# Kernel tuning notes

Hardware: AMD Instinct MI355X
Metric: run time of the kernel (lower is better)

Reference implementation:

```python
import jax, jax.numpy as jnp
import numpy as np

B, T, D, H, HD, E, F, K = 512, 32, 512, 16, 32, 4, 2048, 2
EPS = 1e-5

def gelu_gpt2(x):
    c = np.sqrt(2.0 / np.pi).astype(np.float32)
    return 0.5 * x * (1.0 + jnp.tanh(c * (x + 0.044715 * x ** 3)))

def layernorm(x, g, b):
    m = jnp.mean(x, axis=-1, keepdims=True)
    v = jnp.mean((x - m) ** 2, axis=-1, keepdims=True)
    return (x - m) * jax.lax.rsqrt(v + EPS) * g + b

def setup_inputs() -> dict:
    key = jax.random.key(0)
    ks = jax.random.split(key, 12)
    s = 0.02
    return {
        "x": jax.random.normal(ks[0], (B, T, D), jnp.float32),
        "ln1_g": jnp.ones((D,), jnp.float32), "ln1_b": jnp.zeros((D,), jnp.float32),
        "wq": jax.random.normal(ks[1], (H, D, HD), jnp.float32) * s,
        "wk": jax.random.normal(ks[2], (H, D, HD), jnp.float32) * s,
        "wv": jax.random.normal(ks[3], (H, D, HD), jnp.float32) * s,
        "w_proj": jax.random.normal(ks[4], (D, D), jnp.float32) * s,
        "b_proj": jnp.zeros((D,), jnp.float32),
        "ln2_g": jnp.ones((D,), jnp.float32), "ln2_b": jnp.zeros((D,), jnp.float32),
        "w_gate": jax.random.normal(ks[5], (D, E), jnp.float32) * s,
        "w1": jax.random.normal(ks[6], (E, D, F), jnp.float32) * s,
        "b1": jnp.zeros((E, F), jnp.float32),
        "w2": jax.random.normal(ks[7], (E, F, D), jnp.float32) * s,
        "b2": jnp.zeros((E, D), jnp.float32),
    }

def reference(x, ln1_g, ln1_b, wq, wk, wv, w_proj, b_proj, ln2_g, ln2_b, w_gate, w1, b1, w2, b2):
    # --- multi-head causal attention (dropout = eval-mode identity) ---
    h = layernorm(x, ln1_g, ln1_b)                       # [B,T,D]
    q = jnp.einsum('btd,hde->bhte', h, wq)
    k = jnp.einsum('btd,hde->bhte', h, wk)
    v = jnp.einsum('btd,hde->bhte', h, wv)
    # NOTE: original scales by 1/sqrt(n_embd), not head_size
    wei = jnp.einsum('bhte,bhse->bhts', q, k) / jnp.sqrt(jnp.float32(D))
    mask = jnp.tril(jnp.ones((T, T), bool))
    wei = jnp.where(mask, wei, -jnp.inf)
    wei = jax.nn.softmax(wei, axis=-1)
    att = jnp.einsum('bhts,bhse->bhte', wei, v)          # [B,H,T,HD]
    att = att.transpose(0, 2, 1, 3).reshape(B, T, D)     # concat heads
    x = x + att @ w_proj + b_proj
    # --- mixture of experts FFN ---
    h2 = layernorm(x, ln2_g, ln2_b).reshape(-1, D)       # [N,D]
    logits = h2 @ w_gate                                  # [N,E] raw gate output
    # faithful to original: scalar mean over all logits
    ep = jnp.mean(logits)
    bal_loss = ep * jnp.log(ep + 0.1)
    w_top, sel = jax.lax.top_k(logits, K)                # [N,K]
    w_top = jax.nn.softmax(w_top, axis=-1)
    combine = jnp.sum(w_top[:, :, None] * jax.nn.one_hot(sel, E, dtype=x.dtype), axis=1)  # [N,E]
    mid = gelu_gpt2(jnp.einsum('nd,edf->nef', h2, w1) + b1)   # [N,E,F]
    eout = jnp.einsum('nef,efd->ned', mid, w2) + b2           # [N,E,D]
    moe = jnp.einsum('ne,ned->nd', combine, eout).reshape(B, T, D)
    return (x + moe, bal_loss)
```

## Files before the change

### kernel.cpp

```cpp
#include <hip/hip_runtime.h>

typedef unsigned short ushort;
typedef unsigned int   uint;
typedef short bf16x8 __attribute__((ext_vector_type(8)));
typedef float f32x4  __attribute__((ext_vector_type(4)));

__device__ __forceinline__ float bf2f(ushort u){
  union { uint u; float f; } c; c.u = ((uint)u) << 16; return c.f;
}
__device__ __forceinline__ ushort f2bf(float f){
  union { float f; uint u; } c; c.f = f;
  return (ushort)((c.u + 0x7fffu + ((c.u >> 16) & 1u)) >> 16);
}
__device__ __forceinline__ float wredsum(float v){
  #pragma unroll
  for (int off = 32; off > 0; off >>= 1) v += __shfl_xor(v, off);
  return v;
}
__device__ __forceinline__ void gload16(const void* g, void* l){
  __builtin_amdgcn_global_load_lds((__attribute__((address_space(1))) void*)(void*)g,
                                   (__attribute__((address_space(3))) void*)l, 16, 0, 0);
}

template<bool SPLIT>
__global__ __launch_bounds__(256) void transpose_to_bf16(
    const float* __restrict__ src, ushort* __restrict__ dhi, ushort* __restrict__ dlo,
    int R, int C)
{
  __shared__ float tile[32][33];
  size_t zoff = (size_t)blockIdx.z * R * C;
  src += zoff; dhi += zoff; if (SPLIT) dlo += zoff;
  int c0 = blockIdx.x * 32, r0 = blockIdx.y * 32;
  int tx = threadIdx.x & 31, ty = threadIdx.x >> 5;
  #pragma unroll
  for (int i = 0; i < 32; i += 8)
    tile[ty + i][tx] = src[(size_t)(r0 + ty + i) * C + (c0 + tx)];
  __syncthreads();
  #pragma unroll
  for (int i = 0; i < 32; i += 8){
    float v = tile[tx][ty + i];
    ushort hi = f2bf(v);
    dhi[(size_t)(c0 + ty + i) * R + (r0 + tx)] = hi;
    if constexpr (SPLIT)
      dlo[(size_t)(c0 + ty + i) * R + (r0 + tx)] = f2bf(v - bf2f(hi));
  }
}

__global__ __launch_bounds__(256) void transpose_qkv(
    const float* __restrict__ wq, const float* __restrict__ wk, const float* __restrict__ wv,
    ushort* __restrict__ dhi, ushort* __restrict__ dlo)
{
  __shared__ float tile[32][33];
  int z = blockIdx.z;
  int which = z >> 4, h = z & 15;
  const float* src = (which == 0) ? wq : (which == 1) ? wk : wv;
  size_t soff = (size_t)h * 512 * 32;
  size_t doff = (size_t)which * 262144 + soff;
  src += soff;
  int r0 = blockIdx.y * 32;
  int tx = threadIdx.x & 31, ty = threadIdx.x >> 5;
  #pragma unroll
  for (int i = 0; i < 32; i += 8)
    tile[ty + i][tx] = src[(size_t)(r0 + ty + i) * 32 + tx];
  __syncthreads();
  #pragma unroll
  for (int i = 0; i < 32; i += 8){
    float v = tile[tx][ty + i];
    ushort hi = f2bf(v);
    dhi[doff + (size_t)(ty + i) * 512 + (r0 + tx)] = hi;
    dlo[doff + (size_t)(ty + i) * 512 + (r0 + tx)] = f2bf(v - bf2f(hi));
  }
}

__global__ __launch_bounds__(256) void ln_split(
    const float* __restrict__ x, const float* __restrict__ g, const float* __restrict__ b,
    ushort* __restrict__ hhi, ushort* __restrict__ hlo)
{
  int w = threadIdx.x >> 6, lane = threadIdx.x & 63;
  int row = blockIdx.x * 4 + w;
  const float* xr = x + (size_t)row * 512;
  int d = lane * 8;
  float4 a0 = *(const float4*)(xr + d);
  float4 a1 = *(const float4*)(xr + d + 4);
  float v[8] = {a0.x,a0.y,a0.z,a0.w,a1.x,a1.y,a1.z,a1.w};
  float s = 0.f;
  #pragma unroll
  for (int j = 0; j < 8; j++) s += v[j];
  s = wredsum(s);
  float mean = s * (1.f/512.f);
  float q = 0.f;
  #pragma unroll
  for (int j = 0; j < 8; j++){ float t = v[j] - mean; q += t*t; }
  q = wredsum(q);
  float rstd = rsqrtf(q * (1.f/512.f) + 1e-5f);
  ushort hu[8], lu[8];
  #pragma unroll
  for (int j = 0; j < 8; j++){
    float h = (v[j] - mean) * rstd * g[d+j] + b[d+j];
    ushort hi = f2bf(h);
    hu[j] = hi;
    lu[j] = f2bf(h - bf2f(hi));
  }
  uint4 oh, ol;
  oh.x = (uint)hu[0] | ((uint)hu[1]<<16); oh.y = (uint)hu[2] | ((uint)hu[3]<<16);
  oh.z = (uint)hu[4] | ((uint)hu[5]<<16); oh.w = (uint)hu[6] | ((uint)hu[7]<<16);
  ol.x = (uint)lu[0] | ((uint)lu[1]<<16); ol.y = (uint)lu[2] | ((uint)lu[3]<<16);
  ol.z = (uint)lu[4] | ((uint)lu[5]<<16); ol.w = (uint)lu[6] | ((uint)lu[7]<<16);
  *(uint4*)(hhi + (size_t)row*512 + d) = oh;
  *(uint4*)(hlo + (size_t)row*512 + d) = ol;
}

template<int EP>
__global__ __launch_bounds__(256) void gemm_bt(
    const ushort* __restrict__ A, const ushort* __restrict__ Alo,
    const ushort* __restrict__ B, const ushort* __restrict__ Blo,
    int M, int N, int K,
    float* __restrict__ outF,
    const float* __restrict__ bias, const float* __restrict__ resid)
{
  __shared__ __align__(16) ushort As[2][128*32];
  __shared__ __align__(16) ushort Bs[2][128*32];
  const int tid  = threadIdx.x;
  const int lane = tid & 63;
  const int w    = tid >> 6;
  const int wm   = w >> 1, wn = w & 1;
  const int bm   = blockIdx.x, bn = blockIdx.y;

  const int    srow = w*16 + (lane >> 2);
  const int    scol = (lane & 3) * 8;
  const size_t aoff = (size_t)(bm*128 + srow) * K + scol;
  const size_t boff = (size_t)(bn*128 + srow) * K + scol;
  const int lbase0 = (w*16) * 32;
  const int lbase1 = (64 + w*16) * 32;

  f32x4 acc[4][4];
  #pragma unroll
  for (int i = 0; i < 4; i++)
    #pragma unroll
    for (int j = 0; j < 4; j++) acc[i][j] = f32x4{0.f,0.f,0.f,0.f};

  const int nk = K >> 5;
  for (int kt = 0; kt < nk; ++kt) {
    const size_t ko = (size_t)kt * 32;
    gload16(A + aoff + ko,               &As[0][lbase0]);
    gload16(A + aoff + (size_t)64*K + ko,&As[0][lbase1]);
    gload16(B + boff + ko,               &Bs[0][lbase0]);
    gload16(B + boff + (size_t)64*K + ko,&Bs[0][lbase1]);
    gload16(Alo + aoff + ko,               &As[1][lbase0]);
    gload16(Alo + aoff + (size_t)64*K + ko,&As[1][lbase1]);
    gload16(Blo + boff + ko,               &Bs[1][lbase0]);
    gload16(Blo + boff + (size_t)64*K + ko,&Bs[1][lbase1]);
    __syncthreads();

    bf16x8 ah[4], bh[4], al[4], bl[4];
    const int kk = (lane >> 4) * 8;
    const int ar = wm*64 + (lane & 15);
    const int br = wn*64 + (lane & 15);
    #pragma unroll
    for (int i = 0; i < 4; i++){
      ah[i] = *(const bf16x8*)&As[0][(ar + i*16)*32 + kk];
      bh[i] = *(const bf16x8*)&Bs[0][(br + i*16)*32 + kk];
      al[i] = *(const bf16x8*)&As[1][(ar + i*16)*32 + kk];
      bl[i] = *(const bf16x8*)&Bs[1][(br + i*16)*32 + kk];
    }
    #pragma unroll
    for (int i = 0; i < 4; i++)
      #pragma unroll
      for (int j = 0; j < 4; j++){
        acc[i][j] = __builtin_amdgcn_mfma_f32_16x16x32_bf16(ah[i], bh[j], acc[i][j], 0,0,0);
        acc[i][j] = __builtin_amdgcn_mfma_f32_16x16x32_bf16(ah[i], bl[j], acc[i][j], 0,0,0);
        acc[i][j] = __builtin_amdgcn_mfma_f32_16x16x32_bf16(al[i], bh[j], acc[i][j], 0,0,0);
      }
    __syncthreads();
  }

  const int r0 = bm*128 + wm*64;
  const int c0 = bn*128 + wn*64;
  const int cl = lane & 15;
  const int rl = (lane >> 4) * 4;
  #pragma unroll
  for (int i = 0; i < 4; i++){
    #pragma unroll
    for (int r = 0; r < 4; r++){
      const int row = r0 + i*16 + rl + r;
      #pragma unroll
      for (int j = 0; j < 4; j++){
        const int col = c0 + j*16 + cl;
        float v = acc[i][j][r];
        size_t idx = (size_t)row * N + col;
        if constexpr (EP == 0) outF[idx] = v;
        else                   outF[idx] = v + bias[col] + resid[idx];
      }
    }
  }
}

__global__ __launch_bounds__(256) void gemm_w1(
    const ushort* __restrict__ A, const ushort* __restrict__ Ball,
    const float* __restrict__ biasAll, ushort* __restrict__ midOut,
    const int* __restrict__ list, const int* __restrict__ seg)
{
  constexpr int K = 512, N = 2048, NBN = 16;
  __shared__ __align__(16) ushort LB[128*132];
  const int tid = threadIdx.x, lane = tid & 63, w = tid >> 6;
  const int wm = w >> 1, wn = w & 1;

  const int nloc = gridDim.x >> 3;
  const int lid  = (blockIdx.x & 7) * nloc + (blockIdx.x >> 3);
  const int bm   = lid / NBN, bn = lid % NBN;
  if (bm >= seg[4]) return;
  int e = 0;
  while (bm >= seg[e+1]) e++;
  const int ltile = bm - seg[e];
  const int* listE = list + e*16384;

  const int jrows = w * 32;
  const int lrow  = lane >> 3;
  const int lgcol = (((lane & 7) ^ lrow)) * 8;

  size_t asrc[4], bsrc[4];
  const ushort* Bm = Ball + (size_t)e * N * K;
  #pragma unroll
  for (int j = 0; j < 4; j++){
    int ar8 = jrows + j*8 + lrow;
    int tok = listE[ltile*128 + ar8];
    asrc[j] = (size_t)tok * K + lgcol;
    bsrc[j] = (size_t)(bn*128 + ar8) * K + lgcol;
  }

  f32x4 acc[4][4];
  #pragma unroll
  for (int i = 0; i < 4; i++)
    #pragma unroll
    for (int j = 0; j < 4; j++) acc[i][j] = f32x4{0.f,0.f,0.f,0.f};

  const int ar = wm*64 + (lane & 15);
  const int br = wn*64 + (lane & 15);
  const int rsw = lane & 7;

  #pragma unroll
  for (int kt = 0; kt < (K >> 6); ++kt){
    const size_t k0 = (size_t)kt * 64;
    #pragma unroll
    for (int j = 0; j < 4; j++){
      gload16(A  + asrc[j] + k0, &LB[(jrows + j*8)*64]);
      gload16(Bm + bsrc[j] + k0, &LB[8192 + (jrows + j*8)*64]);
    }
    __syncthreads();
    #pragma unroll
    for (int ks = 0; ks < 2; ++ks){
      const int g    = ks*4 + (lane >> 4);
      const int goff = (g ^ rsw) * 8;
      bf16x8 af[4], bfr[4];
      #pragma unroll
      for (int i = 0; i < 4; i++){
        af[i]  = *(const bf16x8*)&LB[(ar + i*16)*64 + goff];
        bfr[i] = *(const bf16x8*)&LB[8192 + (br + i*16)*64 + goff];
      }
      #pragma unroll
      for (int i = 0; i < 4; i++)
        #pragma unroll
        for (int j = 0; j < 4; j++)
          acc[i][j] = __builtin_amdgcn_mfma_f32_16x16x32_bf16(af[i], bfr[j], acc[i][j], 0,0,0);
    }
    __syncthreads();
  }

  const int cl = lane & 15;
  const int rl = (lane >> 4) * 4;
  float bj[4];
  #pragma unroll
  for (int j = 0; j < 4; j++)
    bj[j] = biasAll[e*N + bn*128 + wn*64 + j*16 + cl];
  #pragma unroll
  for (int i = 0; i < 4; i++){
    #pragma unroll
    for (int j = 0; j < 4; j++){
      const int cc = wn*64 + j*16 + cl;
      #pragma unroll
      for (int r = 0; r < 4; r++){
        const int rloc = wm*64 + i*16 + rl + r;
        float t = acc[i][j][r] + bj[j];
        float u2 = 1.5957691216057308f * (t + 0.044715f * t*t*t);
        float ex = __expf(u2);
        float gl = t - t * __builtin_amdgcn_rcpf(ex + 1.f);
        LB[rloc*132 + cc] = f2bf(gl);
      }
    }
  }
  __syncthreads();
  const int ch = tid & 15;
  #pragma unroll
  for (int it = 0; it < 8; ++it){
    const int rr = (tid >> 4) + it*16;
    bf16x8 v = *(const bf16x8*)&LB[rr*132 + ch*8];
    *(bf16x8*)&midOut[(size_t)(bm*128 + rr)*2048 + bn*128 + ch*8] = v;
  }
}

__global__ __launch_bounds__(256) void gemm_w2(
    const ushort* __restrict__ mid, const ushort* __restrict__ Ball,
    const float* __restrict__ biasAll, ushort* __restrict__ eout,
    const int* __restrict__ seg)
{
  constexpr int K = 2048, N = 512, NBN = 4;
  __shared__ __align__(16) ushort LB[4*128*64];
  const int tid = threadIdx.x, lane = tid & 63, w = tid >> 6;
  const int wm = w >> 1, wn = w & 1;

  const int nloc = gridDim.x >> 3;
  const int lid  = (blockIdx.x & 7) * nloc + (blockIdx.x >> 3);
  const int bm   = lid / NBN, bn = lid % NBN;
  if (bm >= seg[4]) return;
  int e = 0;
  while (bm >= seg[e+1]) e++;

  const int jrows = w * 32;
  const int lrow  = lane >> 3;
  const int lgcol = (((lane & 7) ^ lrow)) * 8;

  size_t asrc[4], bsrc[4];
  const ushort* Bm = Ball + (size_t)e * N * K;
  #pragma unroll
  for (int j = 0; j < 4; j++){
    int ar8 = jrows + j*8 + lrow;
    asrc[j] = (size_t)(bm*128 + ar8) * K + lgcol;
    bsrc[j] = (size_t)(bn*128 + ar8) * K + lgcol;
  }

  f32x4 acc[4][4];
  #pragma unroll
  for (int i = 0; i < 4; i++)
    #pragma unroll
    for (int j = 0; j < 4; j++) acc[i][j] = f32x4{0.f,0.f,0.f,0.f};

  constexpr int nk = K >> 6;

  #pragma unroll
  for (int j = 0; j < 4; j++){
    gload16(mid + asrc[j], &LB[(jrows + j*8)*64]);
    gload16(Bm  + bsrc[j], &LB[16384 + (jrows + j*8)*64]);
  }

  const int ar = wm*64 + (lane & 15);
  const int br = wn*64 + (lane & 15);
  const int rsw = lane & 7;

  for (int kt = 0; kt < nk; ++kt){
    const int cur  = kt & 1;
    const int curA = cur * 8192;
    const int curB = 16384 + cur * 8192;
    if (kt + 1 < nk){
      const int nxtA = (cur ^ 1) * 8192;
      const int nxtB = 16384 + (cur ^ 1) * 8192;
      const size_t k0 = (size_t)(kt + 1) * 64;
      #pragma unroll
      for (int j = 0; j < 4; j++){
        gload16(mid + asrc[j] + k0, &LB[nxtA + (jrows + j*8)*64]);
        gload16(Bm  + bsrc[j] + k0, &LB[nxtB + (jrows + j*8)*64]);
      }
      asm volatile("s_waitcnt vmcnt(8)" ::: "memory");
    } else {
      asm volatile("s_waitcnt vmcnt(0)" ::: "memory");
    }
    __builtin_amdgcn_s_barrier();
    __builtin_amdgcn_sched_barrier(0);
    #pragma unroll
    for (int ks = 0; ks < 2; ++ks){
      const int g    = ks*4 + (lane >> 4);
      const int goff = (g ^ rsw) * 8;
      bf16x8 af[4], bfr[4];
      #pragma unroll
      for (int i = 0; i < 4; i++){
        af[i]  = *(const bf16x8*)&LB[curA + (ar + i*16)*64 + goff];
        bfr[i] = *(const bf16x8*)&LB[curB + (br + i*16)*64 + goff];
      }
      #pragma unroll
      for (int i = 0; i < 4; i++)
        #pragma unroll
        for (int j = 0; j < 4; j++)
          acc[i][j] = __builtin_amdgcn_mfma_f32_16x16x32_bf16(af[i], bfr[j], acc[i][j], 0,0,0);
    }
    __builtin_amdgcn_sched_barrier(0);
    asm volatile("" ::: "memory");
    __builtin_amdgcn_s_barrier();
  }

  const int cl = lane & 15;
  const int rl = (lane >> 4) * 4;
  float bj[4];
  #pragma unroll
  for (int j = 0; j < 4; j++)
    bj[j] = biasAll[e*N + bn*128 + wn*64 + j*16 + cl];
  #pragma unroll
  for (int i = 0; i < 4; i++){
    #pragma unroll
    for (int j = 0; j < 4; j++){
      const int cc = wn*64 + j*16 + cl;
      #pragma unroll
      for (int r = 0; r < 4; r++){
        const int rloc = wm*64 + i*16 + rl + r;
        LB[rloc*132 + cc] = f2bf(acc[i][j][r] + bj[j]);
      }
    }
  }
  __syncthreads();
  const int ch = tid & 15;
  #pragma unroll
  for (int it = 0; it < 8; ++it){
    const int rr = (tid >> 4) + it*16;
    bf16x8 v = *(const bf16x8*)&LB[rr*132 + ch*8];
    *(bf16x8*)&eout[(size_t)(bm*128 + rr)*512 + bn*128 + ch*8] = v;
  }
}

__global__ __launch_bounds__(256) void moe_combine(
    const ushort* __restrict__ eout, const int2* __restrict__ rowSlots,
    const float2* __restrict__ wts, float* __restrict__ out)
{
  int w = threadIdx.x >> 6, lane = threadIdx.x & 63;
  int row = blockIdx.x * 4 + w;
  int2 rs = rowSlots[row];
  float2 wv = wts[row];
  int d = lane * 8;
  uint4 u0 = *(const uint4*)(eout + (size_t)rs.x*512 + d);
  uint4 u1 = *(const uint4*)(eout + (size_t)rs.y*512 + d);
  float* op = out + (size_t)row*512 + d;
  float4 o0 = *(float4*)op;
  float4 o1 = *(float4*)(op + 4);
  o0.x += wv.x*bf2f((ushort)u0.x)        + wv.y*bf2f((ushort)u1.x);
  o0.y += wv.x*bf2f((ushort)(u0.x>>16))  + wv.y*bf2f((ushort)(u1.x>>16));
  o0.z += wv.x*bf2f((ushort)u0.y)        + wv.y*bf2f((ushort)u1.y);
  o0.w += wv.x*bf2f((ushort)(u0.y>>16))  + wv.y*bf2f((ushort)(u1.y>>16));
  o1.x += wv.x*bf2f((ushort)u0.z)        + wv.y*bf2f((ushort)u1.z);
  o1.y += wv.x*bf2f((ushort)(u0.z>>16))  + wv.y*bf2f((ushort)(u1.z>>16));
  o1.z += wv.x*bf2f((ushort)u0.w)        + wv.y*bf2f((ushort)u1.w);
  o1.w += wv.x*bf2f((ushort)(u0.w>>16))  + wv.y*bf2f((ushort)(u1.w>>16));
  *(float4*)op       = o0;
  *(float4*)(op + 4) = o1;
}

__global__ __launch_bounds__(64) void attn32(
    const float* __restrict__ qkv, ushort* __restrict__ atthi, ushort* __restrict__ attlo)
{
  int bh = blockIdx.x; int b = bh >> 4, h = bh & 15;
  __shared__ float qs[32][33], ks[32][33], vs[32][33], ps[32][33];
  int lane = threadIdx.x;
  int t = lane >> 1, cb = (lane & 1) * 16;
  const float* src = qkv + (size_t)(b*32 + t)*1536 + h*32 + cb;
  #pragma unroll
  for (int j = 0; j < 16; j += 4){
    float4 q4 = *(const float4*)(src + j);
    float4 k4 = *(const float4*)(src + 512 + j);
    float4 v4 = *(const float4*)(src + 1024 + j);
    qs[t][cb+j]=q4.x; qs[t][cb+j+1]=q4.y; qs[t][cb+j+2]=q4.z; qs[t][cb+j+3]=q4.w;
    ks[t][cb+j]=k4.x; ks[t][cb+j+1]=k4.y; ks[t][cb+j+2]=k4.z; ks[t][cb+j+3]=k4.w;
    vs[t][cb+j]=v4.x; vs[t][cb+j+1]=v4.y; vs[t][cb+j+2]=v4.z; vs[t][cb+j+3]=v4.w;
  }
  __syncthreads();
  const float scale = 0.044194173824159216f;
  float sc[16];
  #pragma unroll
  for (int j = 0; j < 16; j++){
    int c = cb + j;
    if (c <= t) {
      float d = 0.f;
      #pragma unroll
      for (int i = 0; i < 32; i++) d += qs[t][i] * ks[c][i];
      sc[j] = d * scale;
    } else sc[j] = -1e30f;
  }
  float mx = -1e30f;
  #pragma unroll
  for (int j = 0; j < 16; j++) mx = fmaxf(mx, sc[j]);
  mx = fmaxf(mx, __shfl_xor(mx, 1));
  float p[16], sum = 0.f;
  #pragma unroll
  for (int j = 0; j < 16; j++){
    int c = cb + j;
    if (c <= t) { p[j] = expf(sc[j] - mx); sum += p[j]; } else p[j] = 0.f;
  }
  sum += __shfl_xor(sum, 1);
  float inv = 1.f / sum;
  #pragma unroll
  for (int j = 0; j < 16; j++) ps[t][cb+j] = p[j] * inv;
  __syncthreads();
  float o[16];
  #pragma unroll
  for (int j = 0; j < 16; j++) o[j] = 0.f;
  for (int s2 = 0; s2 <= t; ++s2){
    float wv = ps[t][s2];
    #pragma unroll
    for (int j = 0; j < 16; j++) o[j] += wv * vs[s2][cb+j];
  }
  size_t base = (size_t)(b*32 + t)*512 + h*32 + cb;
  ushort hu[16], lu[16];
  #pragma unroll
  for (int j = 0; j < 16; j++){
    ushort hi = f2bf(o[j]);
    hu[j] = hi; lu[j] = f2bf(o[j] - bf2f(hi));
  }
  uint4 oh0, oh1, ol0, ol1;
  oh0.x=(uint)hu[0]|((uint)hu[1]<<16);  oh0.y=(uint)hu[2]|((uint)hu[3]<<16);
  oh0.z=(uint)hu[4]|((uint)hu[5]<<16);  oh0.w=(uint)hu[6]|((uint)hu[7]<<16);
  oh1.x=(uint)hu[8]|((uint)hu[9]<<16);  oh1.y=(uint)hu[10]|((uint)hu[11]<<16);
  oh1.z=(uint)hu[12]|((uint)hu[13]<<16);oh1.w=(uint)hu[14]|((uint)hu[15]<<16);
  ol0.x=(uint)lu[0]|((uint)lu[1]<<16);  ol0.y=(uint)lu[2]|((uint)lu[3]<<16);
  ol0.z=(uint)lu[4]|((uint)lu[5]<<16);  ol0.w=(uint)lu[6]|((uint)lu[7]<<16);
  ol1.x=(uint)lu[8]|((uint)lu[9]<<16);  ol1.y=(uint)lu[10]|((uint)lu[11]<<16);
  ol1.z=(uint)lu[12]|((uint)lu[13]<<16);ol1.w=(uint)lu[14]|((uint)lu[15]<<16);
  *(uint4*)(atthi + base)     = oh0;  *(uint4*)(atthi + base + 8) = oh1;
  *(uint4*)(attlo + base)     = ol0;  *(uint4*)(attlo + base + 8) = ol1;
}

__global__ __launch_bounds__(256) void ln2_gate(
    const float* __restrict__ x1, const float* __restrict__ g, const float* __restrict__ b,
    const float* __restrict__ wgate, ushort* __restrict__ h2,
    int* __restrict__ selp, float2* __restrict__ wts,
    int* __restrict__ blockCnt, float* __restrict__ partials)
{
  __shared__ float wsumLds[4];
  __shared__ int   selLds[4];
  int w = threadIdx.x >> 6, lane = threadIdx.x & 63;
  int row = blockIdx.x * 4 + w;
  const float* xr = x1 + (size_t)row * 512;
  int d = lane * 8;
  float4 a0 = *(const float4*)(xr + d);
  float4 a1 = *(const float4*)(xr + d + 4);
  float v[8] = {a0.x,a0.y,a0.z,a0.w,a1.x,a1.y,a1.z,a1.w};
  float s = 0.f;
  #pragma unroll
  for (int j = 0; j < 8; j++) s += v[j];
  s = wredsum(s);
  float mean = s * (1.f/512.f);
  float q = 0.f;
  #pragma unroll
  for (int j = 0; j < 8; j++){ float t = v[j] - mean; q += t*t; }
  q = wredsum(q);
  float rstd = rsqrtf(q * (1.f/512.f) + 1e-5f);
  float acc0=0.f, acc1=0.f, acc2=0.f, acc3=0.f;
  ushort hu[8];
  #pragma unroll
  for (int j = 0; j < 8; j++){
    float h = (v[j] - mean) * rstd * g[d+j] + b[d+j];
    hu[j] = f2bf(h);
    float4 wgv = *(const float4*)(wgate + (size_t)(d+j)*4);
    acc0 += h * wgv.x; acc1 += h * wgv.y; acc2 += h * wgv.z; acc3 += h * wgv.w;
  }
  uint4 oh;
  oh.x=(uint)hu[0]|((uint)hu[1]<<16); oh.y=(uint)hu[2]|((uint)hu[3]<<16);
  oh.z=(uint)hu[4]|((uint)hu[5]<<16); oh.w=(uint)hu[6]|((uint)hu[7]<<16);
  *(uint4*)(h2 + (size_t)row*512 + d) = oh;
  acc0 = wredsum(acc0); acc1 = wredsum(acc1); acc2 = wredsum(acc2); acc3 = wredsum(acc3);
  if (lane == 0){
    float l[4] = {acc0, acc1, acc2, acc3};
    int i0 = 0;
    for (int e = 1; e < 4; e++) if (l[e] > l[i0]) i0 = e;
    int i1 = -1;
    for (int e = 0; e < 4; e++){ if (e == i0) continue; if (i1 < 0 || l[e] > l[i1]) i1 = e; }
    float e1 = expf(l[i1] - l[i0]);
    float w1v = e1 / (1.f + e1), w0v = 1.f / (1.f + e1);
    int packed = i0 | (i1 << 8);
    selp[row] = packed;
    wts[row]  = make_float2(w0v, w1v);
    selLds[w] = packed;
    wsumLds[w] = l[0] + l[1] + l[2] + l[3];
  }
  __syncthreads();
  if (threadIdx.x < 4){
    int e = threadIdx.x, c = 0;
    #pragma unroll
    for (int i = 0; i < 4; i++){
      int sp = selLds[i];
      c += ((sp & 0xff) == e) + (((sp >> 8) & 0xff) == e);
    }
    blockCnt[e*4096 + blockIdx.x] = c;
  }
  if (threadIdx.x == 0)
    partials[blockIdx.x] = wsumLds[0] + wsumLds[1] + wsumLds[2] + wsumLds[3];
}

__global__ __launch_bounds__(256) void scan_offsets(
    const int* __restrict__ blockCnt, int* __restrict__ blockOff,
    int* __restrict__ cnt, int* __restrict__ seg,
    const float* __restrict__ partials, float* __restrict__ lossOut)
{
  __shared__ int cntL[4];
  __shared__ float ws4[4];
  int w = threadIdx.x >> 6, lane = threadIdx.x & 63;
  const int* src = blockCnt + w*4096;
  int* dst = blockOff + w*4096;
  int off = 0;
  for (int i = 0; i < 4096; i += 64){
    int v = src[i + lane];
    int orig = v;
    #pragma unroll
    for (int dlt = 1; dlt < 64; dlt <<= 1){
      int t = __shfl_up(v, dlt);
      if (lane >= dlt) v += t;
    }
    dst[i + lane] = off + v - orig;
    off += __shfl(v, 63);
  }
  if (lane == 0){ cnt[w] = off; cntL[w] = off; }
  __syncthreads();
  if (threadIdx.x == 0){
    int t = 0;
    for (int e = 0; e < 4; e++){ seg[e] = t; t += (cntL[e] + 127) >> 7; }
    seg[4] = t;
  }
  float s = 0.f;
  for (int i = threadIdx.x; i < 4096; i += 256) s += partials[i];
  s = wredsum(s);
  if ((threadIdx.x & 63) == 0) ws4[threadIdx.x >> 6] = s;
  __syncthreads();
  if (threadIdx.x == 0){
    float tot = ws4[0] + ws4[1] + ws4[2] + ws4[3];
    float ep = tot * (1.f/65536.f);
    lossOut[0] = ep * logf(ep + 0.1f);
  }
}

__global__ __launch_bounds__(256) void route_write(
    const int* __restrict__ selp, const int* __restrict__ blockOff,
    const int* __restrict__ seg, int* __restrict__ list, int2* __restrict__ rowSlots)
{
  int row = blockIdx.x * 256 + threadIdx.x;
  int g = row & ~3;
  int b = row >> 2;
  int my = selp[row];
  int e0 = my & 0xff, e1 = (my >> 8) & 0xff;
  int r0 = 0, r1 = 0;
  for (int r = g; r < row; ++r){
    int sp = selp[r];
    int a = sp & 0xff, c = (sp >> 8) & 0xff;
    r0 += (a == e0) + (c == e0);
    r1 += (a == e1) + (c == e1);
  }
  int slot0 = blockOff[e0*4096 + b] + r0;
  int slot1 = blockOff[e1*4096 + b] + r1;
  list[e0*16384 + slot0] = row;
  list[e1*16384 + slot1] = row;
  rowSlots[row] = make_int2(seg[e0]*128 + slot0, seg[e1]*128 + slot1);
}

extern "C" void kernel_launch(void* const* d_in, const int* in_sizes, int n_in,
                              void* d_out, int out_size, void* d_ws, size_t ws_size,
                              hipStream_t stream)
{
  const float* x     = (const float*)d_in[0];
  const float* ln1g  = (const float*)d_in[1];
  const float* ln1b  = (const float*)d_in[2];
  const float* wq    = (const float*)d_in[3];
  const float* wk    = (const float*)d_in[4];
  const float* wv    = (const float*)d_in[5];
  const float* wproj = (const float*)d_in[6];
  const float* bproj = (const float*)d_in[7];
  const float* ln2g  = (const float*)d_in[8];
  const float* ln2b  = (const float*)d_in[9];
  const float* wgate = (const float*)d_in[10];
  const float* w1    = (const float*)d_in[11];
  const float* b1    = (const float*)d_in[12];
  const float* w2    = (const float*)d_in[13];
  const float* b2    = (const float*)d_in[14];
  float* out = (float*)d_out;

  char* ws = (char*)d_ws;
  ushort* hHi   = (ushort*)(ws + 0);
  ushort* hLo   = (ushort*)(ws + 16777216);
  ushort* qkvTh = (ushort*)(ws + 33554432);
  ushort* qkvTl = (ushort*)(ws + 35127296);
  ushort* pTh   = (ushort*)(ws + 36700160);
  ushort* pTl   = (ushort*)(ws + 37224448);
  float*  qkvF  = (float*)(ws + 37748736);
  ushort* attHi = (ushort*)(ws + 138412032);
  ushort* attLo = (ushort*)(ws + 155189248);
  ushort* mid   = (ushort*)(ws + 0);
  ushort* eout  = (ushort*)(ws + 137183744);
  ushort* h2    = (ushort*)(ws + 171966464);
  ushort* w1T   = (ushort*)(ws + 188743680);
  ushort* w2T   = (ushort*)(ws + 197132288);
  char* rb = ws + 136314880;
  int*    cnt      = (int*)   (rb + 0);
  int*    seg      = (int*)   (rb + 256);
  int*    list     = (int*)   (rb + 512);
  int2*   rowSlots = (int2*)  (rb + 262656);
  float*  partials = (float*) (rb + 524800);
  int*    selp     = (int*)   (rb + 541184);
  float2* wts      = (float2*)(rb + 606720);
  int*    blockCnt = (int*)   (rb + 737792);
  int*    blockOff = (int*)   (rb + 803328);

  transpose_qkv<<<dim3(1,16,48), 256, 0, stream>>>(wq, wk, wv, qkvTh, qkvTl);
  transpose_to_bf16<true ><<<dim3(16,16,1), 256, 0, stream>>>(wproj, pTh, pTl, 512, 512);
  transpose_to_bf16<false><<<dim3(64,16,4), 256, 0, stream>>>(w1, w1T, nullptr, 512, 2048);
  transpose_to_bf16<false><<<dim3(16,64,4), 256, 0, stream>>>(w2, w2T, nullptr, 2048, 512);

  ln_split<<<dim3(4096), 256, 0, stream>>>(x, ln1g, ln1b, hHi, hLo);

  gemm_bt<0><<<dim3(128,12), 256, 0, stream>>>(hHi, hLo, qkvTh, qkvTl,
      16384, 1536, 512, qkvF, nullptr, nullptr);

  attn32<<<dim3(8192), 64, 0, stream>>>(qkvF, attHi, attLo);

  gemm_bt<1><<<dim3(128,4), 256, 0, stream>>>(attHi, attLo, pTh, pTl,
      16384, 512, 512, out, bproj, x);

  (void)hipMemsetAsync(list, 0, 4*16384*sizeof(int), stream);
  ln2_gate<<<dim3(4096), 256, 0, stream>>>(out, ln2g, ln2b, wgate, h2, selp, wts, blockCnt, partials);
  scan_offsets<<<dim3(1), 256, 0, stream>>>(blockCnt, blockOff, cnt, seg, partials, out + 8388608);
  route_write<<<dim3(64), 256, 0, stream>>>(selp, blockOff, seg, list, rowSlots);

  gemm_w1<<<dim3(4160), 256, 0, stream>>>(h2,  w1T, b1, mid,  list, seg);
  gemm_w2<<<dim3(1040), 256, 0, stream>>>(mid, w2T, b2, eout, seg);
  moe_combine<<<dim3(4096), 256, 0, stream>>>(eout, rowSlots, wts, out);
}
```

Baseline: 466.0 us.

## Widen expert GEMM tiles to 128x256 for w1 and w2

gemm_w1 now computes a 128x256 output tile per 256-thread block, with each wave holding a 4x8 MFMA accumulator set. The epilogue is staged through LDS in two halves. gemm_w2 moves to 512 threads with a 128x256 tile, double-buffered B tiles twice as large, and an adjusted vmcnt wait. The aim is to raise arithmetic intensity and cut redundant reloads of A rows (gathered tokens) across N-tiles, at the cost of more registers and LDS per block, fewer blocks, and a serialized two-pass epilogue.

After: 595.0 us. +27.7%, slower.

```diff
diff --git a/kernel.cpp b/kernel.cpp
--- a/kernel.cpp
+++ b/kernel.cpp
@@ -200,53 +200,178 @@
     const float* __restrict__ biasAll, ushort* __restrict__ midOut,
     const int* __restrict__ list, const int* __restrict__ seg)
 {
-  constexpr int K = 512, N = 2048, NBN = 16;
-  __shared__ __align__(16) ushort LB[128*132];
+  constexpr int K = 512, N = 2048, NBT = 8;
+  __shared__ __align__(16) ushort LB[24576];
   const int tid = threadIdx.x, lane = tid & 63, w = tid >> 6;
   const int wm = w >> 1, wn = w & 1;
 
   const int nloc = gridDim.x >> 3;
   const int lid  = (blockIdx.x & 7) * nloc + (blockIdx.x >> 3);
-  const int bm   = lid / NBN, bn = lid % NBN;
+  const int bm   = lid / NBT, bn = lid % NBT;
   if (bm >= seg[4]) return;
   int e = 0;
   while (bm >= seg[e+1]) e++;
   const int ltile = bm - seg[e];
   const int* listE = list + e*16384;
 
-  const int jrows = w * 32;
   const int lrow  = lane >> 3;
-  const int lgcol = (((lane & 7) ^ lrow)) * 8;
-
-  size_t asrc[4], bsrc[4];
+  const int lgcol = ((lane & 7) ^ lrow) * 8;
+
+  size_t asrc[4], bsrc[8];
   const ushort* Bm = Ball + (size_t)e * N * K;
   #pragma unroll
   for (int j = 0; j < 4; j++){
-    int ar8 = jrows + j*8 + lrow;
+    int ar8 = w*32 + j*8 + lrow;
     int tok = listE[ltile*128 + ar8];
     asrc[j] = (size_t)tok * K + lgcol;
-    bsrc[j] = (size_t)(bn*128 + ar8) * K + lgcol;
-  }
-
-  f32x4 acc[4][4];
+  }
+  #pragma unroll
+  for (int j = 0; j < 8; j++){
+    int br8 = w*64 + j*8 + lrow;
+    bsrc[j] = (size_t)(bn*256 + br8) * K + lgcol;
+  }
+
+  f32x4 acc[4][8];
   #pragma unroll
   for (int i = 0; i < 4; i++)
     #pragma unroll
-    for (int j = 0; j < 4; j++) acc[i][j] = f32x4{0.f,0.f,0.f,0.f};
-
-  const int ar = wm*64 + (lane & 15);
-  const int br = wn*64 + (lane & 15);
+    for (int j = 0; j < 8; j++) acc[i][j] = f32x4{0.f,0.f,0.f,0.f};
+
+  const int ar  = wm*64 + (lane & 15);
+  const int brb = (lane & 15);
   const int rsw = lane & 7;
 
-  #pragma unroll
   for (int kt = 0; kt < (K >> 6); ++kt){
     const size_t k0 = (size_t)kt * 64;
     #pragma unroll
-    for (int j = 0; j < 4; j++){
-      gload16(A  + asrc[j] + k0, &LB[(jrows + j*8)*64]);
-      gload16(Bm + bsrc[j] + k0, &LB[8192 + (jrows + j*8)*64]);
-    }
+    for (int j = 0; j < 4; j++) gload16(A  + asrc[j] + k0, &LB[(w*32 + j*8)*64]);
+    #pragma unroll
+    for (int j = 0; j < 8; j++) gload16(Bm + bsrc[j] + k0, &LB[8192 + (w*64 + j*8)*64]);
     __syncthreads();
+    #pragma unroll
+    for (int ks = 0; ks < 2; ++ks){
+      const int g    = ks*4 + (lane >> 4);
+      const int goff = (g ^ rsw) * 8;
+      bf16x8 af[4], bfr[8];
+      #pragma unroll
+      for (int i = 0; i < 4; i++) af[i]  = *(const bf16x8*)&LB[(ar + i*16)*64 + goff];
+      #pragma unroll
+      for (int j = 0; j < 8; j++) bfr[j] = *(const bf16x8*)&LB[8192 + (wn*128 + brb + j*16)*64 + goff];
+      #pragma unroll
+      for (int i = 0; i < 4; i++)
+        #pragma unroll
+        for (int j = 0; j < 8; j++)
+          acc[i][j] = __builtin_amdgcn_mfma_f32_16x16x32_bf16(af[i], bfr[j], acc[i][j], 0,0,0);
+    }
+    __syncthreads();
+  }
+
+  const int cl = lane & 15;
+  const int rl = (lane >> 4) * 4;
+  float bj[8];
+  #pragma unroll
+  for (int j = 0; j < 8; j++)
+    bj[j] = biasAll[e*N + bn*256 + wn*128 + j*16 + cl];
+  const int ch = tid & 15;
+  #pragma unroll
+  for (int p = 0; p < 2; ++p){
+    if (wn == p){
+      #pragma unroll
+      for (int i = 0; i < 4; i++){
+        #pragma unroll
+        for (int j = 0; j < 8; j++){
+          const int cc = j*16 + cl;
+          #pragma unroll
+          for (int r = 0; r < 4; r++){
+            const int rloc = wm*64 + i*16 + rl + r;
+            float t = acc[i][j][r] + bj[j];
+            float u2 = 1.5957691216057308f * (t + 0.044715f * t*t*t);
+            float ex = __expf(u2);
+            float gl = t - t * __builtin_amdgcn_rcpf(ex + 1.f);
+            LB[rloc*132 + cc] = f2bf(gl);
+          }
+        }
+      }
+    }
+    __syncthreads();
+    #pragma unroll
+    for (int it = 0; it < 8; ++it){
+      const int rr = (tid >> 4) + it*16;
+      bf16x8 v = *(const bf16x8*)&LB[rr*132 + ch*8];
+      *(bf16x8*)&midOut[(size_t)(bm*128 + rr)*2048 + bn*256 + p*128 + ch*8] = v;
+    }
+    __syncthreads();
+  }
+}
+
+__global__ __launch_bounds__(512) void gemm_w2(
+    const ushort* __restrict__ mid, const ushort* __restrict__ Ball,
+    const float* __restrict__ biasAll, ushort* __restrict__ eout,
+    const int* __restrict__ seg)
+{
+  constexpr int K = 2048, N = 512, NBT = 2;
+  __shared__ __align__(16) ushort LB[49152];
+  const int tid = threadIdx.x, lane = tid & 63, w = tid >> 6;
+  const int wm = w >> 2, wn = w & 3;
+
+  const int nloc = gridDim.x >> 3;
+  const int lid  = (blockIdx.x & 7) * nloc + (blockIdx.x >> 3);
+  const int bm   = lid / NBT, bn = lid % NBT;
+  if (bm >= seg[4]) return;
+  int e = 0;
+  while (bm >= seg[e+1]) e++;
+
+  const int lrow  = lane >> 3;
+  const int lgcol = ((lane & 7) ^ lrow) * 8;
+
+  size_t asrc[2], bsrc[4];
+  const ushort* Bm = Ball + (size_t)e * N * K;
+  #pragma unroll
+  for (int j = 0; j < 2; j++){
+    int ar8 = w*16 + j*8 + lrow;
+    asrc[j] = (size_t)(bm*128 + ar8) * K + lgcol;
+  }
+  #pragma unroll
+  for (int j = 0; j < 4; j++){
+    int br8 = w*32 + j*8 + lrow;
+    bsrc[j] = (size_t)(bn*256 + br8) * K + lgcol;
+  }
+
+  f32x4 acc[4][4];
+  #pragma unroll
+  for (int i = 0; i < 4; i++)
+    #pragma unroll
+    for (int j = 0; j < 4; j++) acc[i][j] = f32x4{0.f,0.f,0.f,0.f};
+
+  constexpr int nk = K >> 6;
+
+  #pragma unroll
+  for (int j = 0; j < 2; j++) gload16(mid + asrc[j], &LB[(w*16 + j*8)*64]);
+  #pragma unroll
+  for (int j = 0; j < 4; j++) gload16(Bm  + bsrc[j], &LB[16384 + (w*32 + j*8)*64]);
+
+  const int ar  = wm*64 + (lane & 15);
+  const int brb = wn*64 + (lane & 15);
+  const int rsw = lane & 7;
+
+  for (int kt = 0; kt < nk; ++kt){
+    const int cur  = kt & 1;
+    const int curA = cur * 8192;
+    const int curB = 16384 + cur * 16384;
+    if (kt + 1 < nk){
+      const int nxtA = (cur ^ 1) * 8192;
+      const int nxtB = 16384 + (cur ^ 1) * 16384;
+      const size_t k0 = (size_t)(kt + 1) * 64;
+      #pragma unroll
+      for (int j = 0; j < 2; j++) gload16(mid + asrc[j] + k0, &LB[nxtA + (w*16 + j*8)*64]);
+      #pragma unroll
+      for (int j = 0; j < 4; j++) gload16(Bm  + bsrc[j] + k0, &LB[nxtB + (w*32 + j*8)*64]);
+      asm volatile("s_waitcnt vmcnt(6)" ::: "memory");
+    } else {
+      asm volatile("s_waitcnt vmcnt(0)" ::: "memory");
+    }
+    __builtin_amdgcn_s_barrier();
+    __builtin_amdgcn_sched_barrier(0);
     #pragma unroll
     for (int ks = 0; ks < 2; ++ks){
       const int g    = ks*4 + (lane >> 4);
@@ -254,8 +379,8 @@
       bf16x8 af[4], bfr[4];
       #pragma unroll
       for (int i = 0; i < 4; i++){
-        af[i]  = *(const bf16x8*)&LB[(ar + i*16)*64 + goff];
-        bfr[i] = *(const bf16x8*)&LB[8192 + (br + i*16)*64 + goff];
+        af[i]  = *(const bf16x8*)&LB[curA + (ar + i*16)*64 + goff];
+        bfr[i] = *(const bf16x8*)&LB[curB + (brb + i*16)*64 + goff];
       }
       #pragma unroll
       for (int i = 0; i < 4; i++)
@@ -263,7 +388,9 @@
         for (int j = 0; j < 4; j++)
           acc[i][j] = __builtin_amdgcn_mfma_f32_16x16x32_bf16(af[i], bfr[j], acc[i][j], 0,0,0);
     }
-    __syncthreads();
+    __builtin_amdgcn_sched_barrier(0);
+    asm volatile("" ::: "memory");
+    __builtin_amdgcn_s_barrier();
   }
 
   const int cl = lane & 15;
@@ -271,146 +398,32 @@
   float bj[4];
   #pragma unroll
   for (int j = 0; j < 4; j++)
-    bj[j] = biasAll[e*N + bn*128 + wn*64 + j*16 + cl];
-  #pragma unroll
-  for (int i = 0; i < 4; i++){
-    #pragma unroll
-    for (int j = 0; j < 4; j++){
-      const int cc = wn*64 + j*16 + cl;
-      #pragma unroll
-      for (int r = 0; r < 4; r++){
-        const int rloc = wm*64 + i*16 + rl + r;
-        float t = acc[i][j][r] + bj[j];
-        float u2 = 1.5957691216057308f * (t + 0.044715f * t*t*t);
-        float ex = __expf(u2);
-        float gl = t - t * __builtin_amdgcn_rcpf(ex + 1.f);
-        LB[rloc*132 + cc] = f2bf(gl);
+    bj[j] = biasAll[e*N + bn*256 + wn*64 + j*16 + cl];
+  const int ch = tid & 15;
+  #pragma unroll
+  for (int p = 0; p < 2; ++p){
+    if ((wn >> 1) == p){
+      #pragma unroll
+      for (int i = 0; i < 4; i++){
+        #pragma unroll
+        for (int j = 0; j < 4; j++){
+          const int cc = (wn & 1)*64 + j*16 + cl;
+          #pragma unroll
+          for (int r = 0; r < 4; r++){
+            const int rloc = wm*64 + i*16 + rl + r;
+            LB[rloc*132 + cc] = f2bf(acc[i][j][r] + bj[j]);
+          }
+        }
       }
     }
-  }
-  __syncthreads();
-  const int ch = tid & 15;
-  #pragma unroll
-  for (int it = 0; it < 8; ++it){
-    const int rr = (tid >> 4) + it*16;
-    bf16x8 v = *(const bf16x8*)&LB[rr*132 + ch*8];
-    *(bf16x8*)&midOut[(size_t)(bm*128 + rr)*2048 + bn*128 + ch*8] = v;
-  }
-}
-
-__global__ __launch_bounds__(256) void gemm_w2(
-    const ushort* __restrict__ mid, const ushort* __restrict__ Ball,
-    const float* __restrict__ biasAll, ushort* __restrict__ eout,
-    const int* __restrict__ seg)
-{
-  constexpr int K = 2048, N = 512, NBN = 4;
-  __shared__ __align__(16) ushort LB[4*128*64];
-  const int tid = threadIdx.x, lane = tid & 63, w = tid >> 6;
-  const int wm = w >> 1, wn = w & 1;
-
-  const int nloc = gridDim.x >> 3;
-  const int lid  = (blockIdx.x & 7) * nloc + (blockIdx.x >> 3);
-  const int bm   = lid / NBN, bn = lid % NBN;
-  if (bm >= seg[4]) return;
-  int e = 0;
-  while (bm >= seg[e+1]) e++;
-
-  const int jrows = w * 32;
-  const int lrow  = lane >> 3;
-  const int lgcol = (((lane & 7) ^ lrow)) * 8;
-
-  size_t asrc[4], bsrc[4];
-  const ushort* Bm = Ball + (size_t)e * N * K;
-  #pragma unroll
-  for (int j = 0; j < 4; j++){
-    int ar8 = jrows + j*8 + lrow;
-    asrc[j] = (size_t)(bm*128 + ar8) * K + lgcol;
-    bsrc[j] = (size_t)(bn*128 + ar8) * K + lgcol;
-  }
-
-  f32x4 acc[4][4];
-  #pragma unroll
-  for (int i = 0; i < 4; i++)
-    #pragma unroll
-    for (int j = 0; j < 4; j++) acc[i][j] = f32x4{0.f,0.f,0.f,0.f};
-
-  constexpr int nk = K >> 6;
-
-  #pragma unroll
-  for (int j = 0; j < 4; j++){
-    gload16(mid + asrc[j], &LB[(jrows + j*8)*64]);
-    gload16(Bm  + bsrc[j], &LB[16384 + (jrows + j*8)*64]);
-  }
-
-  const int ar = wm*64 + (lane & 15);
-  const int br = wn*64 + (lane & 15);
-  const int rsw = lane & 7;
-
-  for (int kt = 0; kt < nk; ++kt){
-    const int cur  = kt & 1;
-    const int curA = cur * 8192;
-    const int curB = 16384 + cur * 8192;
-    if (kt + 1 < nk){
-      const int nxtA = (cur ^ 1) * 8192;
-      const int nxtB = 16384 + (cur ^ 1) * 8192;
-      const size_t k0 = (size_t)(kt + 1) * 64;
-      #pragma unroll
-      for (int j = 0; j < 4; j++){
-        gload16(mid + asrc[j] + k0, &LB[nxtA + (jrows + j*8)*64]);
-        gload16(Bm  + bsrc[j] + k0, &LB[nxtB + (jrows + j*8)*64]);
-      }
-      asm volatile("s_waitcnt vmcnt(8)" ::: "memory");
-    } else {
-      asm volatile("s_waitcnt vmcnt(0)" ::: "memory");
-    }
-    __builtin_amdgcn_s_barrier();
-    __builtin_amdgcn_sched_barrier(0);
-    #pragma unroll
-    for (int ks = 0; ks < 2; ++ks){
-      const int g    = ks*4 + (lane >> 4);
-      const int goff = (g ^ rsw) * 8;
-      bf16x8 af[4], bfr[4];
-      #pragma unroll
-      for (int i = 0; i < 4; i++){
-        af[i]  = *(const bf16x8*)&LB[curA + (ar + i*16)*64 + goff];
-        bfr[i] = *(const bf16x8*)&LB[curB + (br + i*16)*64 + goff];
-      }
-      #pragma unroll
-      for (int i = 0; i < 4; i++)
-        #pragma unroll
-        for (int j = 0; j < 4; j++)
-          acc[i][j] = __builtin_amdgcn_mfma_f32_16x16x32_bf16(af[i], bfr[j], acc[i][j], 0,0,0);
-    }
-    __builtin_amdgcn_sched_barrier(0);
-    asm volatile("" ::: "memory");
-    __builtin_amdgcn_s_barrier();
-  }
-
-  const int cl = lane & 15;
-  const int rl = (lane >> 4) * 4;
-  float bj[4];
-  #pragma unroll
-  for (int j = 0; j < 4; j++)
-    bj[j] = biasAll[e*N + bn*128 + wn*64 + j*16 + cl];
-  #pragma unroll
-  for (int i = 0; i < 4; i++){
-    #pragma unroll
-    for (int j = 0; j < 4; j++){
-      const int cc = wn*64 + j*16 + cl;
-      #pragma unroll
-      for (int r = 0; r < 4; r++){
-        const int rloc = wm*64 + i*16 + rl + r;
-        LB[rloc*132 + cc] = f2bf(acc[i][j][r] + bj[j]);
-      }
-    }
-  }
-  __syncthreads();
-  const int ch = tid & 15;
-  #pragma unroll
-  for (int it = 0; it < 8; ++it){
-    const int rr = (tid >> 4) + it*16;
-    bf16x8 v = *(const bf16x8*)&LB[rr*132 + ch*8];
-    *(bf16x8*)&eout[(size_t)(bm*128 + rr)*512 + bn*128 + ch*8] = v;
+    __syncthreads();
+    #pragma unroll
+    for (int it = 0; it < 4; ++it){
+      const int rr = (tid >> 4) + it*32;
+      bf16x8 v = *(const bf16x8*)&LB[rr*132 + ch*8];
+      *(bf16x8*)&eout[(size_t)(bm*128 + rr)*512 + bn*256 + p*128 + ch*8] = v;
+    }
+    __syncthreads();
   }
 }
 
@@ -711,7 +724,7 @@
   scan_offsets<<<dim3(1), 256, 0, stream>>>(blockCnt, blockOff, cnt, seg, partials, out + 8388608);
   route_write<<<dim3(64), 256, 0, stream>>>(selp, blockOff, seg, list, rowSlots);
 
-  gemm_w1<<<dim3(4160), 256, 0, stream>>>(h2,  w1T, b1, mid,  list, seg);
-  gemm_w2<<<dim3(1040), 256, 0, stream>>>(mid, w2T, b2, eout, seg);
+  gemm_w1<<<dim3(2080), 256, 0, stream>>>(h2,  w1T, b1, mid,  list, seg);
+  gemm_w2<<<dim3(520), 512, 0, stream>>>(mid, w2T, b2, eout, seg);
   moe_combine<<<dim3(4096), 256, 0, stream>>>(eout, rowSlots, wts, out);
 }
```
